# Kernel tuning notes

Measured on AMD Instinct MI355X. Metric: run time of the kernel, lower is better.

The kernel has to match this reference:

```python
import jax, jax.numpy as jnp
import numpy as np


def setup_inputs() -> dict:
    key = jax.random.key(0)
    ks = jax.random.split(key, 8)
    B, H, W = 4, 1024, 1024
    F_, Nuv = 40000, 25000
    Ht, Wt = 1024, 1024
    # pytorch3d-style globally packed face indices: pixel of batch b holds idx in [b*F, (b+1)*F) or -1
    local = jax.random.randint(ks[0], (B, H, W, 1), 0, F_)
    covered = jax.random.uniform(ks[1], (B, H, W, 1)) < 0.8
    offset = (jnp.arange(B) * F_)[:, None, None, None]
    pix_to_face = jnp.where(covered, local + offset, -1).astype(jnp.int64)
    bary = jax.random.uniform(ks[2], (B, H, W, 1, 3), dtype=jnp.float32)
    bary = bary / jnp.sum(bary, axis=-1, keepdims=True)
    uvmap = jax.random.normal(ks[3], (B, 3, Ht, Wt), dtype=jnp.float32)
    vertex_uv = jax.random.uniform(ks[4], (Nuv, 2), dtype=jnp.float32)
    face_uv = jax.random.randint(ks[5], (F_, 3), 0, Nuv).astype(jnp.int64)
    bkg_color = jnp.zeros((3,), jnp.float32)
    return {"bary_coords": bary, "uvmap": uvmap, "vertex_uv": vertex_uv,
            "bkg_color": bkg_color, "pix_to_face": pix_to_face,
            "face_uv": face_uv, "num_faces": F_}


def _bilinear_sample(tex, u, v):
    # tex: [B,C,Ht,Wt]; u,v: [B,H,W] in pixel coords (align_corners=True), border padding
    B, C, Ht, Wt = tex.shape
    u = jnp.clip(u, 0.0, Wt - 1.0)
    v = jnp.clip(v, 0.0, Ht - 1.0)
    x0 = jnp.floor(u)
    y0 = jnp.floor(v)
    x0i = x0.astype(jnp.int32)
    y0i = y0.astype(jnp.int32)
    x1i = jnp.minimum(x0i + 1, Wt - 1)
    y1i = jnp.minimum(y0i + 1, Ht - 1)
    wx = (u - x0)[..., None]
    wy = (v - y0)[..., None]
    bidx = jnp.arange(B)[:, None, None]
    g = lambda yi, xi: tex[bidx, :, yi, xi]  # [B,H,W,C]
    top = g(y0i, x0i) * (1.0 - wx) + g(y0i, x1i) * wx
    bot = g(y1i, x0i) * (1.0 - wx) + g(y1i, x1i) * wx
    return top * (1.0 - wy) + bot * wy  # [B,H,W,C]


def reference(bary_coords, uvmap, vertex_uv, bkg_color, pix_to_face, face_uv, num_faces):
    B, H, W, K = pix_to_face.shape
    Ht, Wt = uvmap.shape[2], uvmap.shape[3]
    # vertex_uv with v flipped, as in forward(): stack((u, 1-v))
    vt = jnp.stack([vertex_uv[:, 0], 1.0 - vertex_uv[:, 1]], axis=1)  # [Nuv,2]
    face_vt = vt[face_uv]  # [F,3,2]
    pf = pix_to_face[..., 0]  # [B,H,W] globally packed indices
    valid = pf != -1
    # unpack global -> per-batch local face index (invalid pixels -> 0, masked later)
    local = jnp.where(valid, pf - jnp.arange(B, dtype=pf.dtype)[:, None, None] * num_faces, 0)
    uv_tri = face_vt[local]  # [B,H,W,3,2]
    # barycentric interpolation of the 3 vertex uvs
    uv = jnp.einsum('bhwk,bhwkc->bhwc', bary_coords[:, :, :, 0, :], uv_tri)  # [B,H,W,2]
    sampled = _bilinear_sample(uvmap, uv[..., 0] * (Wt - 1), uv[..., 1] * (Ht - 1))  # [B,H,W,3]
    render = jnp.transpose(sampled, (0, 3, 1, 2))  # [B,3,H,W]
    is_valid = valid[:, None, :, :].astype(render.dtype)  # [B,1,H,W]
    render = render * is_valid + bkg_color[None, :, None, None] * (1.0 - is_valid)
    return render, is_valid
```

## Files before the change

kernel.cpp:

```cpp
#include <hip/hip_runtime.h>
#include <hip/hip_fp16.h>


#define BB    4
#define HWT   (1 << 20)
#define WMASK 1023
#define HHALF (HWT / 2)

static __device__ __forceinline__ unsigned h2b(float a, float b) {
    __half2 h = __floats2half2_rn(a, b);
    return *reinterpret_cast<const unsigned*>(&h);
}
static __device__ __forceinline__ float2 h2f(unsigned u) {
    return __half22float2(*reinterpret_cast<const __half2*>(&u));
}

__global__ __launch_bounds__(256) void build_ftab(
    const int* __restrict__ face_uv, const float* __restrict__ vertex_uv,
    float4* __restrict__ ftab, int F)
{
    const int f = blockIdx.x * blockDim.x + threadIdx.x;
    if (f >= F) return;
    const int i0 = face_uv[f * 3 + 0];
    const int i1 = face_uv[f * 3 + 1];
    const int i2 = face_uv[f * 3 + 2];
    float4 a, b;
    a.x = vertex_uv[i0 * 2 + 0]; a.y = 1.0f - vertex_uv[i0 * 2 + 1];
    a.z = vertex_uv[i1 * 2 + 0]; a.w = 1.0f - vertex_uv[i1 * 2 + 1];
    b.x = vertex_uv[i2 * 2 + 0]; b.y = 1.0f - vertex_uv[i2 * 2 + 1];
    b.z = 0.0f; b.w = 0.0f;
    ftab[f * 2 + 0] = a;
    ftab[f * 2 + 1] = b;
}

template <bool PAD32>
__global__ __launch_bounds__(256) void pack_quad_chunk(
    const float* __restrict__ uvmap, unsigned* __restrict__ ptexu, int b0)
{
    const int t = blockIdx.x * blockDim.x + threadIdx.x;
    const int b  = b0 + (t >> 20);
    const int hw = t & (HWT - 1);
    const int i  = (b << 20) | hw;
    const int x  = hw & WMASK;
    const int y  = hw >> 10;
    const int xr = min(x + 1, WMASK);
    const int yd = min(y + 1, WMASK);
    const float* base = uvmap + ((size_t)b * 3 << 20);
    const int iTL = (y  << 10) | x,  iTR = (y  << 10) | xr;
    const int iBL = (yd << 10) | x,  iBR = (yd << 10) | xr;
    const float c0TL = base[iTL],           c0TR = base[iTR];
    const float c1TL = base[HWT + iTL],     c1TR = base[HWT + iTR];
    const float c2TL = base[2 * HWT + iTL], c2TR = base[2 * HWT + iTR];
    const float c0BL = base[iBL],           c0BR = base[iBR];
    const float c1BL = base[HWT + iBL],     c1BR = base[HWT + iBR];
    const float c2BL = base[2 * HWT + iBL], c2BR = base[2 * HWT + iBR];

    const unsigned t0 = h2b(c0TL, c1TL), t1 = h2b(c2TL, c0TR), t2 = h2b(c1TR, c2TR);
    const unsigned u0 = h2b(c0BL, c1BL), u1 = h2b(c2BL, c0BR), u2 = h2b(c1BR, c2BR);

    if (PAD32) {
        uint4* p = reinterpret_cast<uint4*>(ptexu);
        uint4 a; a.x = t0; a.y = t1; a.z = t2; a.w = 0u;
        uint4 c; c.x = u0; c.y = u1; c.z = u2; c.w = 0u;
        p[(size_t)i * 2 + 0] = a;
        p[(size_t)i * 2 + 1] = c;
    } else {
        const size_t o = (size_t)i * 6;
        ptexu[o + 0] = t0; ptexu[o + 1] = t1; ptexu[o + 2] = t2;
        ptexu[o + 3] = u0; ptexu[o + 4] = u1; ptexu[o + 5] = u2;
    }
}

template <bool PAD32>
__global__ __launch_bounds__(256) void render_chunk(
    const unsigned* __restrict__ ptexu, const float4* __restrict__ ftab,
    const float* __restrict__ bary, const int* __restrict__ pix,
    const float* __restrict__ bkg, int F,
    float* __restrict__ render, float* __restrict__ is_valid, int b0)
{
    const int tid = blockIdx.x * blockDim.x + threadIdx.x;
    const float bkg0 = bkg[0], bkg1 = bkg[1], bkg2 = bkg[2];

    int idx[4], bj[4];
    #pragma unroll
    for (int j = 0; j < 4; ++j) {
        bj[j]  = b0 + (j >> 1);
        idx[j] = (bj[j] << 20) | (tid + ((j & 1) ? HHALF : 0));
    }

    int pf[4];
    #pragma unroll
    for (int j = 0; j < 4; ++j)
        pf[j] = __builtin_nontemporal_load(&pix[idx[j]]);

    float ba[4][3];
    #pragma unroll
    for (int j = 0; j < 4; ++j) {
        const size_t o = (size_t)idx[j] * 3;
        ba[j][0] = __builtin_nontemporal_load(&bary[o + 0]);
        ba[j][1] = __builtin_nontemporal_load(&bary[o + 1]);
        ba[j][2] = __builtin_nontemporal_load(&bary[o + 2]);
    }

    float4 A[4], Bv[4];
    #pragma unroll
    for (int j = 0; j < 4; ++j) {
        const int lf = (pf[j] != -1) ? pf[j] - bj[j] * F : 0;
        A[j]  = ftab[lf * 2 + 0];
        Bv[j] = ftab[lf * 2 + 1];
    }

    unsigned t0[4], t1[4], t2[4], u0[4], u1[4], u2[4];
    float wx[4], wy[4];
    #pragma unroll
    for (int j = 0; j < 4; ++j) {
        const float u = ba[j][0] * A[j].x + ba[j][1] * A[j].z + ba[j][2] * Bv[j].x;
        const float v = ba[j][0] * A[j].y + ba[j][1] * A[j].w + ba[j][2] * Bv[j].y;
        float x = fminf(fmaxf(u * 1023.0f, 0.0f), 1023.0f);
        float y = fminf(fmaxf(v * 1023.0f, 0.0f), 1023.0f);
        if (pf[j] == -1) { x = 0.0f; y = 0.0f; }
        const float xf = floorf(x), yf = floorf(y);
        wx[j] = x - xf; wy[j] = y - yf;
        const int e = (bj[j] << 20) | (((int)yf) << 10) | (int)xf;
        if (PAD32) {
            const uint4* p = reinterpret_cast<const uint4*>(ptexu);
            const uint4 qt = p[(size_t)e * 2 + 0];
            const uint4 qb = p[(size_t)e * 2 + 1];
            t0[j] = qt.x; t1[j] = qt.y; t2[j] = qt.z;
            u0[j] = qb.x; u1[j] = qb.y; u2[j] = qb.z;
        } else {
            const size_t o = (size_t)e * 6;
            t0[j] = ptexu[o + 0]; t1[j] = ptexu[o + 1]; t2[j] = ptexu[o + 2];
            u0[j] = ptexu[o + 3]; u1[j] = ptexu[o + 4]; u2[j] = ptexu[o + 5];
        }
    }

    #pragma unroll
    for (int j = 0; j < 4; ++j) {
        const float2 a01 = h2f(t0[j]), a2b = h2f(t1[j]), a12 = h2f(t2[j]);
        const float2 c01 = h2f(u0[j]), c2b = h2f(u1[j]), c12 = h2f(u2[j]);
        const float iwx = 1.0f - wx[j], iwy = 1.0f - wy[j];
        const float top0 = a01.x * iwx + a2b.y * wx[j];
        const float top1 = a01.y * iwx + a12.x * wx[j];
        const float top2 = a2b.x * iwx + a12.y * wx[j];
        const float bot0 = c01.x * iwx + c2b.y * wx[j];
        const float bot1 = c01.y * iwx + c12.x * wx[j];
        const float bot2 = c2b.x * iwx + c12.y * wx[j];
        float r0 = top0 * iwy + bot0 * wy[j];
        float r1 = top1 * iwy + bot1 * wy[j];
        float r2 = top2 * iwy + bot2 * wy[j];
        float vf = 1.0f;
        if (pf[j] == -1) { r0 = bkg0; r1 = bkg1; r2 = bkg2; vf = 0.0f; }
        const int hwj = idx[j] & (HWT - 1);
        const int ob  = (bj[j] * 3) << 20;
        __builtin_nontemporal_store(r0, &render[ob + hwj]);
        __builtin_nontemporal_store(r1, &render[ob + HWT + hwj]);
        __builtin_nontemporal_store(r2, &render[ob + 2 * HWT + hwj]);
        __builtin_nontemporal_store(vf, &is_valid[idx[j]]);
    }
}

__global__ __launch_bounds__(256) void uvrender_direct(
    const float* __restrict__ bary, const float* __restrict__ uvmap,
    const float* __restrict__ vertex_uv, const float* __restrict__ bkg,
    const int* __restrict__ pix_to_face, const int* __restrict__ face_uv,
    int F, float* __restrict__ render, float* __restrict__ is_valid)
{
    const int total = BB * HWT;
    const float bkg0 = bkg[0], bkg1 = bkg[1], bkg2 = bkg[2];
    for (int idx = blockIdx.x * blockDim.x + threadIdx.x; idx < total;
         idx += gridDim.x * blockDim.x) {
        const int b  = idx >> 20;
        const int hw = idx & (HWT - 1);
        const int pf = pix_to_face[idx];
        float r0 = bkg0, r1 = bkg1, r2 = bkg2, vflag = 0.0f;
        if (pf != -1) {
            vflag = 1.0f;
            const int local = pf - b * F;
            const int i0 = face_uv[local * 3 + 0];
            const int i1 = face_uv[local * 3 + 1];
            const int i2 = face_uv[local * 3 + 2];
            const float b0 = bary[(size_t)idx * 3 + 0];
            const float b1 = bary[(size_t)idx * 3 + 1];
            const float b2 = bary[(size_t)idx * 3 + 2];
            const float u = b0 * vertex_uv[i0 * 2] + b1 * vertex_uv[i1 * 2] +
                            b2 * vertex_uv[i2 * 2];
            const float v = b0 * (1.0f - vertex_uv[i0 * 2 + 1]) +
                            b1 * (1.0f - vertex_uv[i1 * 2 + 1]) +
                            b2 * (1.0f - vertex_uv[i2 * 2 + 1]);
            float x = fminf(fmaxf(u * 1023.0f, 0.0f), 1023.0f);
            float y = fminf(fmaxf(v * 1023.0f, 0.0f), 1023.0f);
            const float xf = floorf(x), yf = floorf(y);
            const int x0 = (int)xf, y0 = (int)yf;
            const int x1 = min(x0 + 1, WMASK), y1 = min(y0 + 1, WMASK);
            const float wxx = x - xf, wyy = y - yf;
            const float iwx = 1.0f - wxx, iwy = 1.0f - wyy;
            const float* texb = uvmap + ((size_t)b * 3 << 20);
            float out[3];
            #pragma unroll
            for (int c = 0; c < 3; ++c) {
                const float* t = texb + ((size_t)c << 20);
                const float t00 = t[(y0 << 10) | x0];
                const float t01 = t[(y0 << 10) | x1];
                const float t10 = t[(y1 << 10) | x0];
                const float t11 = t[(y1 << 10) | x1];
                out[c] = (t00 * iwx + t01 * wxx) * iwy + (t10 * iwx + t11 * wxx) * wyy;
            }
            r0 = out[0]; r1 = out[1]; r2 = out[2];
        }
        const size_t ob = (size_t)b * 3 * HWT + hw;
        __builtin_nontemporal_store(r0, &render[ob]);
        __builtin_nontemporal_store(r1, &render[ob + HWT]);
        __builtin_nontemporal_store(r2, &render[ob + 2 * (size_t)HWT]);
        __builtin_nontemporal_store(vflag, &is_valid[idx]);
    }
}

extern "C" void kernel_launch(void* const* d_in, const int* in_sizes, int n_in,
                              void* d_out, int out_size, void* d_ws, size_t ws_size,
                              hipStream_t stream) {
    const float* bary        = (const float*)d_in[0];
    const float* uvmap       = (const float*)d_in[1];
    const float* vertex_uv   = (const float*)d_in[2];
    const float* bkg         = (const float*)d_in[3];
    const int*   pix_to_face = (const int*)d_in[4];
    const int*   face_uv     = (const int*)d_in[5];
    const int F = in_sizes[5] / 3;

    float* render   = (float*)d_out;
    float* is_valid = (float*)d_out + (size_t)BB * 3 * HWT;

    const size_t Q32_B  = (size_t)BB * HWT * 32;
    const size_t Q24_B  = (size_t)BB * HWT * 24;
    const size_t FTAB_B = (size_t)F * 2 * sizeof(float4);

    if (ws_size >= Q32_B + FTAB_B) {
        unsigned* ptexu = (unsigned*)d_ws;
        float4*   ftab  = (float4*)((char*)d_ws + Q32_B);
        build_ftab<<<(F + 255) / 256, 256, 0, stream>>>(face_uv, vertex_uv, ftab, F);
        for (int c = 0; c < 2; ++c) {
            pack_quad_chunk<true><<<(2 * HWT) / 256, 256, 0, stream>>>(uvmap, ptexu, c * 2);
            render_chunk<true><<<HHALF / 256, 256, 0, stream>>>(
                ptexu, ftab, bary, pix_to_face, bkg, F, render, is_valid, c * 2);
        }
    } else if (ws_size >= Q24_B + FTAB_B) {
        unsigned* ptexu = (unsigned*)d_ws;
        float4*   ftab  = (float4*)((char*)d_ws + Q24_B);
        build_ftab<<<(F + 255) / 256, 256, 0, stream>>>(face_uv, vertex_uv, ftab, F);
        for (int c = 0; c < 2; ++c) {
            pack_quad_chunk<false><<<(2 * HWT) / 256, 256, 0, stream>>>(uvmap, ptexu, c * 2);
            render_chunk<false><<<HHALF / 256, 256, 0, stream>>>(
                ptexu, ftab, bary, pix_to_face, bkg, F, render, is_valid, c * 2);
        }
    } else {
        uvrender_direct<<<2048, 256, 0, stream>>>(
            bary, uvmap, vertex_uv, bkg, pix_to_face, face_uv, F,
            render, is_valid);
    }
}
```

Before: 138.9 us.

## Fuse ftab build with first pack and overlap chunk-0 render with chunk-1 pack

Replaces the five-launch chunked sequence with three launches. The first launch builds the face table and packs chunk 0. The second interleaves chunk-0 render blocks with chunk-1 pack blocks in a 1:4 ratio, so gather-heavy render work overlaps streaming pack work. The third renders chunk 1. Pack stores become nontemporal vector stores. This cuts launch gaps and tail idle time, but the mixed kernel shares occupancy between heterogeneous blocks and nontemporal texture stores may lose L2/MALL reuse for the following render reads.

```diff
diff --git a/kernel.cpp b/kernel.cpp
--- a/kernel.cpp
+++ b/kernel.cpp
@@ -7,6 +7,8 @@
 #define WMASK 1023
 #define HHALF (HWT / 2)
 
+typedef unsigned uint4_ev __attribute__((ext_vector_type(4)));
+
 static __device__ __forceinline__ unsigned h2b(float a, float b) {
     __half2 h = __floats2half2_rn(a, b);
     return *reinterpret_cast<const unsigned*>(&h);
@@ -15,11 +17,11 @@
     return __half22float2(*reinterpret_cast<const __half2*>(&u));
 }
 
-__global__ __launch_bounds__(256) void build_ftab(
-    const int* __restrict__ face_uv, const float* __restrict__ vertex_uv,
+
+static __device__ __forceinline__ void ftab_body(
+    int f, const int* __restrict__ face_uv, const float* __restrict__ vertex_uv,
     float4* __restrict__ ftab, int F)
 {
-    const int f = blockIdx.x * blockDim.x + threadIdx.x;
     if (f >= F) return;
     const int i0 = face_uv[f * 3 + 0];
     const int i1 = face_uv[f * 3 + 1];
@@ -33,11 +35,9 @@
     ftab[f * 2 + 1] = b;
 }
 
-template <bool PAD32>
-__global__ __launch_bounds__(256) void pack_quad_chunk(
-    const float* __restrict__ uvmap, unsigned* __restrict__ ptexu, int b0)
-{
-    const int t = blockIdx.x * blockDim.x + threadIdx.x;
+static __device__ __forceinline__ void pack_body(
+    int t, const float* __restrict__ uvmap, unsigned* __restrict__ ptexu, int b0)
+{
     const int b  = b0 + (t >> 20);
     const int hw = t & (HWT - 1);
     const int i  = (b << 20) | hw;
@@ -55,30 +55,20 @@
     const float c1BL = base[HWT + iBL],     c1BR = base[HWT + iBR];
     const float c2BL = base[2 * HWT + iBL], c2BR = base[2 * HWT + iBR];
 
-    const unsigned t0 = h2b(c0TL, c1TL), t1 = h2b(c2TL, c0TR), t2 = h2b(c1TR, c2TR);
-    const unsigned u0 = h2b(c0BL, c1BL), u1 = h2b(c2BL, c0BR), u2 = h2b(c1BR, c2BR);
-
-    if (PAD32) {
-        uint4* p = reinterpret_cast<uint4*>(ptexu);
-        uint4 a; a.x = t0; a.y = t1; a.z = t2; a.w = 0u;
-        uint4 c; c.x = u0; c.y = u1; c.z = u2; c.w = 0u;
-        p[(size_t)i * 2 + 0] = a;
-        p[(size_t)i * 2 + 1] = c;
-    } else {
-        const size_t o = (size_t)i * 6;
-        ptexu[o + 0] = t0; ptexu[o + 1] = t1; ptexu[o + 2] = t2;
-        ptexu[o + 3] = u0; ptexu[o + 4] = u1; ptexu[o + 5] = u2;
-    }
-}
-
-template <bool PAD32>
-__global__ __launch_bounds__(256) void render_chunk(
-    const unsigned* __restrict__ ptexu, const float4* __restrict__ ftab,
+    uint4_ev qa, qc;
+    qa.x = h2b(c0TL, c1TL); qa.y = h2b(c2TL, c0TR); qa.z = h2b(c1TR, c2TR); qa.w = 0u;
+    qc.x = h2b(c0BL, c1BL); qc.y = h2b(c2BL, c0BR); qc.z = h2b(c1BR, c2BR); qc.w = 0u;
+    uint4_ev* p = reinterpret_cast<uint4_ev*>(ptexu);
+    __builtin_nontemporal_store(qa, &p[(size_t)i * 2 + 0]);
+    __builtin_nontemporal_store(qc, &p[(size_t)i * 2 + 1]);
+}
+
+static __device__ __forceinline__ void render_body(
+    int tid, const unsigned* __restrict__ ptexu, const float4* __restrict__ ftab,
     const float* __restrict__ bary, const int* __restrict__ pix,
     const float* __restrict__ bkg, int F,
     float* __restrict__ render, float* __restrict__ is_valid, int b0)
 {
-    const int tid = blockIdx.x * blockDim.x + threadIdx.x;
     const float bkg0 = bkg[0], bkg1 = bkg[1], bkg2 = bkg[2];
 
     int idx[4], bj[4];
@@ -122,17 +112,11 @@
         const float xf = floorf(x), yf = floorf(y);
         wx[j] = x - xf; wy[j] = y - yf;
         const int e = (bj[j] << 20) | (((int)yf) << 10) | (int)xf;
-        if (PAD32) {
-            const uint4* p = reinterpret_cast<const uint4*>(ptexu);
-            const uint4 qt = p[(size_t)e * 2 + 0];
-            const uint4 qb = p[(size_t)e * 2 + 1];
-            t0[j] = qt.x; t1[j] = qt.y; t2[j] = qt.z;
-            u0[j] = qb.x; u1[j] = qb.y; u2[j] = qb.z;
-        } else {
-            const size_t o = (size_t)e * 6;
-            t0[j] = ptexu[o + 0]; t1[j] = ptexu[o + 1]; t2[j] = ptexu[o + 2];
-            u0[j] = ptexu[o + 3]; u1[j] = ptexu[o + 4]; u2[j] = ptexu[o + 5];
-        }
+        const uint4_ev* p = reinterpret_cast<const uint4_ev*>(ptexu);
+        const uint4_ev qt = p[(size_t)e * 2 + 0];
+        const uint4_ev qb = p[(size_t)e * 2 + 1];
+        t0[j] = qt.x; t1[j] = qt.y; t2[j] = qt.z;
+        u0[j] = qb.x; u1[j] = qb.y; u2[j] = qb.z;
     }
 
     #pragma unroll
@@ -157,6 +141,124 @@
         __builtin_nontemporal_store(r1, &render[ob + HWT + hwj]);
         __builtin_nontemporal_store(r2, &render[ob + 2 * HWT + hwj]);
         __builtin_nontemporal_store(vf, &is_valid[idx[j]]);
+    }
+}
+
+
+__global__ __launch_bounds__(256) void k_ftab_pack0(
+    const int* __restrict__ face_uv, const float* __restrict__ vertex_uv,
+    float4* __restrict__ ftab, const float* __restrict__ uvmap,
+    unsigned* __restrict__ ptexu, int F, int nftab)
+{
+    const int g = blockIdx.x;
+    if (g < nftab) {
+        ftab_body(g * 256 + threadIdx.x, face_uv, vertex_uv, ftab, F);
+    } else {
+        pack_body((g - nftab) * 256 + threadIdx.x, uvmap, ptexu, 0);
+    }
+}
+
+__global__ __launch_bounds__(256) void k_mix(
+    unsigned* __restrict__ ptexu, const float4* __restrict__ ftab,
+    const float* __restrict__ bary, const int* __restrict__ pix,
+    const float* __restrict__ bkg, int F,
+    float* __restrict__ render, float* __restrict__ is_valid,
+    const float* __restrict__ uvmap)
+{
+    const int g = blockIdx.x;
+    const int r = g % 5;
+    if (r == 0) {
+        render_body((g / 5) * 256 + threadIdx.x, ptexu, ftab, bary, pix, bkg, F,
+                    render, is_valid, 0);
+    } else {
+        const int pb = (g / 5) * 4 + (r - 1);
+        pack_body(pb * 256 + threadIdx.x, uvmap, ptexu, 2);
+    }
+}
+
+__global__ __launch_bounds__(256) void k_render1(
+    const unsigned* __restrict__ ptexu, const float4* __restrict__ ftab,
+    const float* __restrict__ bary, const int* __restrict__ pix,
+    const float* __restrict__ bkg, int F,
+    float* __restrict__ render, float* __restrict__ is_valid)
+{
+    render_body(blockIdx.x * 256 + threadIdx.x, ptexu, ftab, bary, pix, bkg, F,
+                render, is_valid, 2);
+}
+
+
+__global__ __launch_bounds__(256) void build_ftab(
+    const int* __restrict__ face_uv, const float* __restrict__ vertex_uv,
+    float4* __restrict__ ftab, int F)
+{
+    ftab_body(blockIdx.x * blockDim.x + threadIdx.x, face_uv, vertex_uv, ftab, F);
+}
+
+__global__ __launch_bounds__(256) void pack_quad24(
+    const float* __restrict__ uvmap, unsigned* __restrict__ ptexu)
+{
+    const int t = blockIdx.x * blockDim.x + threadIdx.x;
+    const int b  = t >> 20;
+    const int hw = t & (HWT - 1);
+    const int x  = hw & WMASK;
+    const int y  = hw >> 10;
+    const int xr = min(x + 1, WMASK);
+    const int yd = min(y + 1, WMASK);
+    const float* base = uvmap + ((size_t)b * 3 << 20);
+    const int iTL = (y  << 10) | x,  iTR = (y  << 10) | xr;
+    const int iBL = (yd << 10) | x,  iBR = (yd << 10) | xr;
+    const size_t o = (size_t)t * 6;
+    ptexu[o + 0] = h2b(base[iTL], base[HWT + iTL]);
+    ptexu[o + 1] = h2b(base[2 * HWT + iTL], base[iTR]);
+    ptexu[o + 2] = h2b(base[HWT + iTR], base[2 * HWT + iTR]);
+    ptexu[o + 3] = h2b(base[iBL], base[HWT + iBL]);
+    ptexu[o + 4] = h2b(base[2 * HWT + iBL], base[iBR]);
+    ptexu[o + 5] = h2b(base[HWT + iBR], base[2 * HWT + iBR]);
+}
+
+__global__ __launch_bounds__(256) void render_quad24(
+    const unsigned* __restrict__ ptexu, const float4* __restrict__ ftab,
+    const float* __restrict__ bary, const int* __restrict__ pix,
+    const float* __restrict__ bkg, int F,
+    float* __restrict__ render, float* __restrict__ is_valid)
+{
+    const int tid = blockIdx.x * blockDim.x + threadIdx.x;
+    const float bkg0 = bkg[0], bkg1 = bkg[1], bkg2 = bkg[2];
+    #pragma unroll
+    for (int j = 0; j < 4; ++j) {
+        const int idx = (j << 20) | tid;
+        const int pf = pix[idx];
+        float r0 = bkg0, r1 = bkg1, r2 = bkg2, vf = 0.0f;
+        if (pf != -1) {
+            vf = 1.0f;
+            const int lf = pf - j * F;
+            const float4 A  = ftab[lf * 2 + 0];
+            const float4 Bv = ftab[lf * 2 + 1];
+            const size_t o = (size_t)idx * 3;
+            const float b0 = bary[o], b1 = bary[o + 1], b2 = bary[o + 2];
+            const float u = b0 * A.x + b1 * A.z + b2 * Bv.x;
+            const float v = b0 * A.y + b1 * A.w + b2 * Bv.y;
+            const float x = fminf(fmaxf(u * 1023.0f, 0.0f), 1023.0f);
+            const float y = fminf(fmaxf(v * 1023.0f, 0.0f), 1023.0f);
+            const float xf = floorf(x), yf = floorf(y);
+            const float wx = x - xf, wy = y - yf;
+            const size_t e = (size_t)((j << 20) | (((int)yf) << 10) | (int)xf) * 6;
+            const float2 a01 = h2f(ptexu[e + 0]);
+            const float2 a2b = h2f(ptexu[e + 1]);
+            const float2 a12 = h2f(ptexu[e + 2]);
+            const float2 c01 = h2f(ptexu[e + 3]);
+            const float2 c2b = h2f(ptexu[e + 4]);
+            const float2 c12 = h2f(ptexu[e + 5]);
+            const float iwx = 1.0f - wx, iwy = 1.0f - wy;
+            r0 = (a01.x * iwx + a2b.y * wx) * iwy + (c01.x * iwx + c2b.y * wx) * wy;
+            r1 = (a01.y * iwx + a12.x * wx) * iwy + (c01.y * iwx + c12.x * wx) * wy;
+            r2 = (a2b.x * iwx + a12.y * wx) * iwy + (c2b.x * iwx + c12.y * wx) * wy;
+        }
+        const int ob = (j * 3) << 20;
+        __builtin_nontemporal_store(r0, &render[ob | tid]);
+        __builtin_nontemporal_store(r1, &render[(ob + HWT) | tid]);
+        __builtin_nontemporal_store(r2, &render[(ob + 2 * HWT) | tid]);
+        __builtin_nontemporal_store(vf, &is_valid[(j << 20) | tid]);
     }
 }
 
@@ -237,21 +339,20 @@
     if (ws_size >= Q32_B + FTAB_B) {
         unsigned* ptexu = (unsigned*)d_ws;
         float4*   ftab  = (float4*)((char*)d_ws + Q32_B);
-        build_ftab<<<(F + 255) / 256, 256, 0, stream>>>(face_uv, vertex_uv, ftab, F);
-        for (int c = 0; c < 2; ++c) {
-            pack_quad_chunk<true><<<(2 * HWT) / 256, 256, 0, stream>>>(uvmap, ptexu, c * 2);
-            render_chunk<true><<<HHALF / 256, 256, 0, stream>>>(
-                ptexu, ftab, bary, pix_to_face, bkg, F, render, is_valid, c * 2);
-        }
+        const int nftab = (F + 255) / 256;
+        k_ftab_pack0<<<nftab + 8192, 256, 0, stream>>>(
+            face_uv, vertex_uv, ftab, uvmap, ptexu, F, nftab);
+        k_mix<<<10240, 256, 0, stream>>>(
+            ptexu, ftab, bary, pix_to_face, bkg, F, render, is_valid, uvmap);
+        k_render1<<<2048, 256, 0, stream>>>(
+            ptexu, ftab, bary, pix_to_face, bkg, F, render, is_valid);
     } else if (ws_size >= Q24_B + FTAB_B) {
         unsigned* ptexu = (unsigned*)d_ws;
         float4*   ftab  = (float4*)((char*)d_ws + Q24_B);
         build_ftab<<<(F + 255) / 256, 256, 0, stream>>>(face_uv, vertex_uv, ftab, F);
-        for (int c = 0; c < 2; ++c) {
-            pack_quad_chunk<false><<<(2 * HWT) / 256, 256, 0, stream>>>(uvmap, ptexu, c * 2);
-            render_chunk<false><<<HHALF / 256, 256, 0, stream>>>(
-                ptexu, ftab, bary, pix_to_face, bkg, F, render, is_valid, c * 2);
-        }
+        pack_quad24<<<(BB * HWT) / 256, 256, 0, stream>>>(uvmap, ptexu);
+        render_quad24<<<HWT / 256, 256, 0, stream>>>(
+            ptexu, ftab, bary, pix_to_face, bkg, F, render, is_valid);
     } else {
         uvrender_direct<<<2048, 256, 0, stream>>>(
             bary, uvmap, vertex_uv, bkg, pix_to_face, face_uv, F,
```

Measured after the change: 168.6 us. 1.21x slower.
